# Kernel tuning notes

Hardware: AMD Instinct MI355X
Metric: run time of the kernel (lower is better)

The kernel has to match this reference:

```python
import jax, jax.numpy as jnp
import numpy as np

D_MODEL = 1024
NUM_HEADS = 16
HEAD_DIM = D_MODEL // NUM_HEADS
B, S = 4, 2048


def _xavier(key, shape, gain=0.1):
    fan_in, fan_out = shape[1], shape[0]
    a = gain * np.sqrt(6.0 / (fan_in + fan_out))
    return jax.random.uniform(key, shape, jnp.float32, -a, a)


def setup_inputs() -> dict:
    key = jax.random.key(0)
    ks = jax.random.split(key, 11)
    inp = {
        "q": jax.random.normal(ks[0], (B, S, D_MODEL), jnp.float32),
        "k": jax.random.normal(ks[1], (B, S, D_MODEL), jnp.float32),
        "v": jax.random.normal(ks[2], (B, S, D_MODEL), jnp.float32),
        # nn.Linear weights are [out, in]; y = x @ W.T + b
        "Wq": _xavier(ks[3], (D_MODEL, D_MODEL)),
        "bq": jnp.zeros((D_MODEL,), jnp.float32),
        "Wk": _xavier(ks[4], (D_MODEL, D_MODEL)),
        "bk": jnp.zeros((D_MODEL,), jnp.float32),
        "Wv": _xavier(ks[5], (D_MODEL, D_MODEL)),
        "bv": jnp.zeros((D_MODEL,), jnp.float32),
        "Wo": _xavier(ks[6], (D_MODEL, D_MODEL)),
        "bo": jnp.zeros((D_MODEL,), jnp.float32),
    }
    return inp


def reference(q, k, v, Wq, bq, Wk, bk, Wv, bv, Wo, bo):
    b = q.shape[0]
    qh = (q @ Wq.T + bq).reshape(b, -1, NUM_HEADS, HEAD_DIM).transpose(0, 2, 1, 3)
    kh = (k @ Wk.T + bk).reshape(b, -1, NUM_HEADS, HEAD_DIM).transpose(0, 2, 1, 3)
    vh = (v @ Wv.T + bv).reshape(b, -1, NUM_HEADS, HEAD_DIM).transpose(0, 2, 1, 3)
    # NOTE: original (buggy) module scales by sqrt(d_model), not sqrt(head_dim)
    scale = 1.0 / jnp.sqrt(jnp.float32(D_MODEL))
    scores = jnp.einsum('bhqd,bhkd->bhqk', qh, kh) * scale  # [B,H,S,S]
    attn = jax.nn.softmax(scores, axis=-1)
    out = jnp.einsum('bhqk,bhkd->bhqd', attn, vh)
    out = out.transpose(0, 2, 1, 3).reshape(b, -1, D_MODEL)
    return out @ Wo.T + bo
```

## Files before the change

kernel.cpp:

```cpp
#include <hip/hip_runtime.h>

typedef unsigned short u16;
typedef short bf16x8 __attribute__((ext_vector_type(8)));
typedef float f32x4 __attribute__((ext_vector_type(4)));
typedef u16 u16x8 __attribute__((ext_vector_type(8)));

__device__ __forceinline__ u16 f2bf(float f) {
  unsigned u = __float_as_uint(f);
  u = u + 0x7fffu + ((u >> 16) & 1u);
  return (u16)(u >> 16);
}

__device__ __forceinline__ float fexp2(float x) {
#if __has_builtin(__builtin_amdgcn_exp2f)
  return __builtin_amdgcn_exp2f(x);
#else
  return exp2f(x);
#endif
}

#define GLD16(ldsp, gp)                                                         \
  __builtin_amdgcn_global_load_lds(                                             \
      (__attribute__((address_space(1))) void*)(void*)(gp),                     \
      (__attribute__((address_space(3))) void*)(ldsp), 16, 0, 0)

#define CVTPK(dst, lo, hi)                                                      \
  asm("v_cvt_pk_bf16_f32 %0, %1, %2" : "=v"(dst) : "v"(lo), "v"(hi))
#define PACK8(dst, a0, a1, a2, a3, a4, a5, a6, a7)                              \
  do {                                                                          \
    union { unsigned u_[4]; bf16x8 v_; } c_;                                    \
    CVTPK(c_.u_[0], a0, a1); CVTPK(c_.u_[1], a2, a3);                           \
    CVTPK(c_.u_[2], a4, a5); CVTPK(c_.u_[3], a6, a7);                           \
    dst = c_.v_;                                                                \
  } while (0)

__global__ __launch_bounds__(256) void pack_w4(const float* __restrict__ w0,
                                               const float* __restrict__ w1,
                                               const float* __restrict__ w2,
                                               const float* __restrict__ w3,
                                               u16* __restrict__ out) {
  int i = blockIdx.x * 256 + threadIdx.x;
  int which = i >> 17;
  const float* src = which == 0 ? w0 : which == 1 ? w1 : which == 2 ? w2 : w3;
  int j = i & 131071;
  const float4* p = (const float4*)src + (size_t)j * 2;
  float4 a = p[0], b = p[1];
  u16x8 r;
  r[0] = f2bf(a.x); r[1] = f2bf(a.y); r[2] = f2bf(a.z); r[3] = f2bf(a.w);
  r[4] = f2bf(b.x); r[5] = f2bf(b.y); r[6] = f2bf(b.z); r[7] = f2bf(b.w);
  *(u16x8*)(out + (size_t)i * 8) = r;
}

__global__ __launch_bounds__(256, 4)
void gemm_qkv(const float* __restrict__ qi, const float* __restrict__ ki,
              const float* __restrict__ vi, const u16* __restrict__ wbf,
              const float* __restrict__ bq, const float* __restrict__ bk,
              const float* __restrict__ bv, u16* __restrict__ qo,
              u16* __restrict__ ko, u16* __restrict__ vo) {
  constexpr int K = 1024;
  __shared__ __align__(16) u16 As[128 * 64];
  __shared__ __align__(16) u16 Bs[128 * 64];
  const int z = blockIdx.z;
  const float* Af = z == 0 ? qi : z == 1 ? ki : vi;
  const u16* Bw = wbf + ((size_t)z << 20);
  const float* bias = z == 0 ? bq : z == 1 ? bk : bv;

  const int t = threadIdx.x;
  const int w = t >> 6, l = t & 63;
  const int lr = l & 15, lg = l >> 4;
  const int flat = blockIdx.x | (blockIdx.y << 3);
  const int swz = ((flat & 7) << 6) | (flat >> 3);
  const int row0 = (swz >> 3) * 128, col0 = (swz & 7) * 128;
  const int wm = (w >> 1) * 64, wn = (w & 1) * 64;

  f32x4 acc[4][4] = {};

  const int ar = t >> 3;
  const int xw = ((t & 7) ^ (ar & 7)) * 16;
  const float* gA = Af + (size_t)(row0 + ar) * K + (t & 7) * 8;
  const u16* gB = Bw + (size_t)(col0 + ar) * K + (((t & 7) ^ (ar & 7)) * 8);
  u16* lB = &Bs[w * 512];

  float4 a0[4], a1[4];
#pragma unroll
  for (int j = 0; j < 4; ++j) {
    const float* p = gA + (size_t)j * 32 * K;
    a0[j] = *(const float4*)p;
    a1[j] = *(const float4*)(p + 4);
  }

  for (int kt = 0; kt < 16; ++kt) {
#pragma unroll
    for (int j = 0; j < 4; ++j)
      GLD16(lB + j * 2048, gB + (size_t)j * 32 * K + kt * 64);
#pragma unroll
    for (int j = 0; j < 4; ++j) {
      bf16x8 c;
      PACK8(c, a0[j].x, a0[j].y, a0[j].z, a0[j].w, a1[j].x, a1[j].y, a1[j].z, a1[j].w);
      *(bf16x8*)((char*)As + (ar + j * 32) * 128 + xw) = c;
    }
    __syncthreads();
    if (kt < 15) {
#pragma unroll
      for (int j = 0; j < 4; ++j) {
        const float* p = gA + (size_t)j * 32 * K + (kt + 1) * 64;
        a0[j] = *(const float4*)p;
        a1[j] = *(const float4*)(p + 4);
      }
    }
#pragma unroll
    for (int kh2 = 0; kh2 < 2; ++kh2) {
      bf16x8 aF[4], bF[4];
      const int bc = (kh2 * 64 + lg * 16) ^ ((lr & 7) * 16);
#pragma unroll
      for (int mi = 0; mi < 4; ++mi)
        aF[mi] = *(const bf16x8*)((const char*)As + (wm + mi * 16 + lr) * 128 + bc);
#pragma unroll
      for (int ni = 0; ni < 4; ++ni)
        bF[ni] = *(const bf16x8*)((const char*)Bs + (wn + ni * 16 + lr) * 128 + bc);
#pragma unroll
      for (int mi = 0; mi < 4; ++mi)
#pragma unroll
        for (int ni = 0; ni < 4; ++ni)
          acc[mi][ni] = __builtin_amdgcn_mfma_f32_16x16x32_bf16(aF[mi], bF[ni],
                                                                acc[mi][ni], 0, 0, 0);
    }
    __syncthreads();
  }

#pragma unroll
  for (int mi = 0; mi < 4; ++mi) {
#pragma unroll
    for (int ni = 0; ni < 4; ++ni) {
      const int n = col0 + wn + ni * 16 + lr;
      const float bvv = bias[n];
#pragma unroll
      for (int r = 0; r < 4; ++r) {
        const int m = row0 + wm + mi * 16 + lg * 4 + r;
        const float vv = acc[mi][ni][r] + bvv;
        const int bI = m >> 11, s = m & 2047, h = n >> 6, d = n & 63;
        if (z == 0) {
          qo[((size_t)((bI << 4) + h) * 2048 + s) * 64 + d] = f2bf(vv * 0.045084223f);
        } else if (z == 1) {
          ko[((size_t)((bI << 4) + h) * 2048 + s) * 64 + d] = f2bf(vv);
        } else {
          int bh = (bI << 4) + h, tile = s >> 6, kp = s & 63;
          int kM = kp >> 5, k5 = kp & 31;
          int kpp = kM * 32 + ((k5 >> 2) & 3) * 8 + (k5 >> 4) * 4 + (k5 & 3);
          int chunk = (kpp >> 3) ^ (d & 7);
          vo[((size_t)bh << 17) + tile * 4096 + d * 64 + chunk * 8 + (kpp & 7)] = f2bf(vv);
        }
      }
    }
  }
}

__global__ __launch_bounds__(256, 3)
void gemm_out(const u16* __restrict__ A, const u16* __restrict__ B,
              const float* __restrict__ bias, float* __restrict__ outp) {
  constexpr int K = 1024;
  __shared__ __align__(16) u16 As[128 * 64];
  __shared__ __align__(16) u16 Bs[128 * 64];
  const int t = threadIdx.x;
  const int w = t >> 6;
  const int l = t & 63;
  const int lr = l & 15, lg = l >> 4;
  const int flat = blockIdx.x | (blockIdx.y << 3);
  const int swz = ((flat & 7) << 6) | (flat >> 3);
  const int row0 = (swz >> 3) * 128, col0 = (swz & 7) * 128;
  const int wm = (w >> 1) * 64, wn = (w & 1) * 64;

  f32x4 acc[4][4] = {};

  const int srow = t >> 3;
  const int scol = ((t & 7) ^ (srow & 7)) * 8;
  const u16* gA = A + (size_t)(row0 + srow) * K + scol;
  const u16* gB = B + (size_t)(col0 + srow) * K + scol;
  u16* lA = &As[w * 512];
  u16* lB = &Bs[w * 512];

  for (int k0 = 0; k0 < K; k0 += 64) {
#pragma unroll
    for (int j = 0; j < 4; ++j) {
      GLD16(lA + j * 2048, gA + (size_t)j * 32 * K + k0);
      GLD16(lB + j * 2048, gB + (size_t)j * 32 * K + k0);
    }
    __syncthreads();
#pragma unroll
    for (int kh2 = 0; kh2 < 2; ++kh2) {
      bf16x8 aF[4], bF[4];
      const int bc = (kh2 * 64 + lg * 16) ^ ((lr & 7) * 16);
#pragma unroll
      for (int mi = 0; mi < 4; ++mi)
        aF[mi] = *(const bf16x8*)((const char*)As + (wm + mi * 16 + lr) * 128 + bc);
#pragma unroll
      for (int ni = 0; ni < 4; ++ni)
        bF[ni] = *(const bf16x8*)((const char*)Bs + (wn + ni * 16 + lr) * 128 + bc);
#pragma unroll
      for (int mi = 0; mi < 4; ++mi)
#pragma unroll
        for (int ni = 0; ni < 4; ++ni)
          acc[mi][ni] = __builtin_amdgcn_mfma_f32_16x16x32_bf16(aF[mi], bF[ni],
                                                                acc[mi][ni], 0, 0, 0);
    }
    __syncthreads();
  }

#pragma unroll
  for (int mi = 0; mi < 4; ++mi)
#pragma unroll
    for (int ni = 0; ni < 4; ++ni) {
      const int n = col0 + wn + ni * 16 + lr;
      const float bv = bias[n];
#pragma unroll
      for (int r = 0; r < 4; ++r) {
        const int m = row0 + wm + mi * 16 + lg * 4 + r;
        outp[(size_t)m * 1024 + n] = acc[mi][ni][r] + bv;
      }
    }
}

#define QKC(KB, D0, D1)                                                         \
  do {                                                                          \
    const char* kb_ = (const char*)(KB);                                        \
    _Pragma("unroll")                                                           \
    for (int cq = 0; cq < 4; ++cq) {                                            \
      const char* rowp_ = kb_ + (cq * 16 + lr) * 128;                           \
      bf16x8 kf0_ = *(const bf16x8*)(rowp_ + xo0);                              \
      bf16x8 kf1_ = *(const bf16x8*)(rowp_ + xo1);                              \
      f32x4 a_ = {}, b_ = {};                                                   \
      a_ = __builtin_amdgcn_mfma_f32_16x16x32_bf16(kf0_, qf[0][0], a_, 0, 0, 0);\
      a_ = __builtin_amdgcn_mfma_f32_16x16x32_bf16(kf1_, qf[0][1], a_, 0, 0, 0);\
      b_ = __builtin_amdgcn_mfma_f32_16x16x32_bf16(kf0_, qf[1][0], b_, 0, 0, 0);\
      b_ = __builtin_amdgcn_mfma_f32_16x16x32_bf16(kf1_, qf[1][1], b_, 0, 0, 0);\
      D0[cq] = a_; D1[cq] = b_;                                                 \
    }                                                                           \
  } while (0)

#define STAGEKV(KSLOT)                                                          \
  do {                                                                          \
    u16* kd_ = &Ks[KSLOT][0] + w * 512;                                         \
    u16* vd_ = &Vl[0][0] + vs * 4096 + w * 512;      \
    GLD16(kd_, gK); GLD16(kd_ + 2048, gK + 2048);                               \
    GLD16(vd_, gV); GLD16(vd_ + 2048, gV + 2048);                               \
    gK += 4096; gV += 4096;                                                     \
  } while (0)

#define SOFTPV(SIN0, SIN1)                                                      \
  do {                                                                          \
    _Pragma("unroll")                                                           \
    for (int cq = 0; cq < 4; ++cq) {                                            \
      _Pragma("unroll")                                                         \
      for (int r = 0; r < 4; ++r) {                                             \
        SIN0[cq][r] = fexp2(SIN0[cq][r]);                                       \
        SIN1[cq][r] = fexp2(SIN1[cq][r]);                                       \
      }                                                                         \
    }                                                                           \
    bf16x8 pA0_, pA1_, pB0_, pB1_;                                              \
    PACK8(pA0_, SIN0[0][0], SIN0[0][1], SIN0[0][2], SIN0[0][3],                 \
                SIN0[1][0], SIN0[1][1], SIN0[1][2], SIN0[1][3]);                \
    PACK8(pA1_, SIN0[2][0], SIN0[2][1], SIN0[2][2], SIN0[2][3],                 \
                SIN0[3][0], SIN0[3][1], SIN0[3][2], SIN0[3][3]);                \
    PACK8(pB0_, SIN1[0][0], SIN1[0][1], SIN1[0][2], SIN1[0][3],                 \
                SIN1[1][0], SIN1[1][1], SIN1[1][2], SIN1[1][3]);                \
    PACK8(pB1_, SIN1[2][0], SIN1[2][1], SIN1[2][2], SIN1[2][3],                 \
                SIN1[3][0], SIN1[3][1], SIN1[3][2], SIN1[3][3]);                \
    sm0 = __builtin_amdgcn_mfma_f32_16x16x32_bf16(pA0_, ones, sm0, 0, 0, 0);    \
    sm0 = __builtin_amdgcn_mfma_f32_16x16x32_bf16(pA1_, ones, sm0, 0, 0, 0);    \
    sm1 = __builtin_amdgcn_mfma_f32_16x16x32_bf16(pB0_, ones, sm1, 0, 0, 0);    \
    sm1 = __builtin_amdgcn_mfma_f32_16x16x32_bf16(pB1_, ones, sm1, 0, 0, 0);    \
    const char* vbb_ = (const char*)(&Vl[0][0] + vu * 4096);     \
    _Pragma("unroll")                                                           \
    for (int dc = 0; dc < 4; ++dc) {                                            \
      const char* rp_ = vbb_ + (dc * 16 + lr) * 128;                            \
      bf16x8 vA_ = *(const bf16x8*)(rp_ + xo0);                                 \
      bf16x8 vB_ = *(const bf16x8*)(rp_ + xo1);                                 \
      o0[dc] = __builtin_amdgcn_mfma_f32_16x16x32_bf16(pA0_, vA_, o0[dc], 0,0,0);\
      o0[dc] = __builtin_amdgcn_mfma_f32_16x16x32_bf16(pA1_, vB_, o0[dc], 0,0,0);\
      o1[dc] = __builtin_amdgcn_mfma_f32_16x16x32_bf16(pB0_, vA_, o1[dc], 0,0,0);\
      o1[dc] = __builtin_amdgcn_mfma_f32_16x16x32_bf16(pB1_, vB_, o1[dc], 0,0,0);\
    }                                                                           \
  } while (0)

__global__ __launch_bounds__(256, 3)
void attn_fwd(const u16* __restrict__ qh, const u16* __restrict__ kh,
              const u16* __restrict__ vp, u16* __restrict__ aout) {
  __shared__ __align__(16) u16 Ks[2][4096];
  __shared__ __align__(16) u16 Vl[3][4096];
  const int t = threadIdx.x;
  const int w = t >> 6, l = t & 63;
  const int lr = l & 15, lg = l >> 4;
  const int flat = blockIdx.x | (blockIdx.y << 4);
  const int swz = ((flat & 7) << 7) | (flat >> 3);
  const int qb = swz & 15, bh = swz >> 4;
  const int q0 = qb * 128 + w * 32;

  bf16x8 qf[2][2];
#pragma unroll
  for (int qi = 0; qi < 2; ++qi) {
    const u16* qp = qh + ((size_t)bh * 2048 + q0 + qi * 16 + lr) * 64 + lg * 8;
    qf[qi][0] = *(const bf16x8*)qp;
    qf[qi][1] = *(const bf16x8*)(qp + 32);
  }

  f32x4 o0[4] = {}, o1[4] = {};
  f32x4 sm0 = {}, sm1 = {};
  const bf16x8 ones = {16256, 16256, 16256, 16256, 16256, 16256, 16256, 16256};

  const int krow = t >> 3, kseg = t & 7;
  const u16* gK = kh + ((size_t)bh * 2048 + krow) * 64 + ((kseg ^ (krow & 7)) * 8);
  const u16* gV = vp + ((size_t)bh << 17) + t * 8;

  const int xo0 = (lg * 16) ^ ((lr & 7) * 16);
  const int xo1 = xo0 ^ 64;

  f32x4 sA0[4], sA1[4], sB0[4], sB1[4];
  int vu = 0, vs = 0;

  STAGEKV(0);
  __syncthreads();
  vs = 1;
  STAGEKV(1);
  QKC(&Ks[0][0], sA0, sA1);
  __syncthreads();
  vs = 2;

  for (int T = 0; T < 32; T += 2) {
    if (T < 30) STAGEKV(0);
    QKC(&Ks[1][0], sB0, sB1);
    SOFTPV(sA0, sA1);
    __syncthreads();
    vu = (vu == 2) ? 0 : vu + 1;
    vs = (vs == 2) ? 0 : vs + 1;

    if (T < 30) STAGEKV(1);
    if (T < 30) QKC(&Ks[0][0], sA0, sA1);
    SOFTPV(sB0, sB1);
    __syncthreads();
    vu = (vu == 2) ? 0 : vu + 1;
    vs = (vs == 2) ? 0 : vs + 1;
  }

  const int b = bh >> 4, h = bh & 15;
#pragma unroll
  for (int r = 0; r < 4; ++r) {
    const float dA = 1.f / sm0[r];
    const float dB = 1.f / sm1[r];
    const size_t rowA = (size_t)b * 2048 + q0 + lg * 4 + r;
#pragma unroll
    for (int dc = 0; dc < 4; ++dc) {
      aout[rowA * 1024 + h * 64 + dc * 16 + lr] = f2bf(o0[dc][r] * dA);
      aout[(rowA + 16) * 1024 + h * 64 + dc * 16 + lr] = f2bf(o1[dc][r] * dB);
    }
  }
}

extern "C" void kernel_launch(void* const* d_in, const int* in_sizes, int n_in,
                              void* d_out, int out_size, void* d_ws, size_t ws_size,
                              hipStream_t stream) {
  const float* q  = (const float*)d_in[0];
  const float* k  = (const float*)d_in[1];
  const float* v  = (const float*)d_in[2];
  const float* Wq = (const float*)d_in[3];
  const float* bq = (const float*)d_in[4];
  const float* Wk = (const float*)d_in[5];
  const float* bk = (const float*)d_in[6];
  const float* Wv = (const float*)d_in[7];
  const float* bv = (const float*)d_in[8];
  const float* Wo = (const float*)d_in[9];
  const float* bo = (const float*)d_in[10];

  char* ws = (char*)d_ws;
  u16* wbf  = (u16*)(ws);
  u16* aout = (u16*)(ws + (8ull << 20));
  u16* qhB  = (u16*)(ws + (24ull << 20));
  u16* khB  = (u16*)(ws + (40ull << 20));
  u16* vtB  = (u16*)(ws + (56ull << 20));

  pack_w4<<<2048, 256, 0, stream>>>(Wq, Wk, Wv, Wo, wbf);
  gemm_qkv<<<dim3(8, 64, 3), 256, 0, stream>>>(q, k, v, wbf, bq, bk, bv,
                                               qhB, khB, vtB);
  attn_fwd<<<dim3(16, 64), 256, 0, stream>>>(qhB, khB, vtB, aout);
  gemm_out<<<dim3(8, 64), 256, 0, stream>>>(aout, wbf + (3u << 20), bo,
                                            (float*)d_out);

  (void)in_sizes; (void)n_in; (void)out_size; (void)ws_size;
}
```

Baseline: 172.7 us.

## Triple-buffer K/V with explicit vmcnt waits and MFMA priority boosts

Replaces the two-slot K / three-slot V rotation, which issued the next tile's QK^T ahead of the softmax-PV step, with a uniform three-slot K/V ring. Each iteration prefetches two tiles ahead and waits with a partial s_waitcnt vmcnt before a raw s_barrier, instead of a full __syncthreads drain. It also raises wave priority around the MFMA blocks with s_setprio and drops the cross-iteration QK software pipelining. The aim is to overlap global-to-LDS loads with compute and cut barrier stalls, at the cost of more LDS per block and less ILP between QK and PV.

```diff
diff --git a/kernel.cpp b/kernel.cpp
--- a/kernel.cpp
+++ b/kernel.cpp
@@ -220,9 +220,27 @@
     }
 }
 
-#define QKC(KB, D0, D1)                                                         \
+#define STG(SLOT)                                                               \
   do {                                                                          \
-    const char* kb_ = (const char*)(KB);                                        \
+    u16* kd_ = &Ks[SLOT][0] + w * 512;                                          \
+    u16* vd_ = &Vl[SLOT][0] + w * 512;                                          \
+    GLD16(kd_, gK); GLD16(kd_ + 2048, gK + 2048);                               \
+    GLD16(vd_, gV); GLD16(vd_ + 2048, gV + 2048);                               \
+    gK += 4096; gV += 4096;                                                     \
+  } while (0)
+
+#define WAITBAR(VMSTR)                                                          \
+  do {                                                                          \
+    asm volatile("s_waitcnt " VMSTR ::: "memory");                              \
+    __builtin_amdgcn_s_barrier();                                               \
+    __builtin_amdgcn_sched_barrier(0);                                          \
+  } while (0)
+
+#define BODYC(S)                                                                \
+  do {                                                                          \
+    const char* kb_ = (const char*)&Ks[S][0];                                   \
+    f32x4 s0_[4], s1_[4];                                                       \
+    __builtin_amdgcn_s_setprio(1);                                              \
     _Pragma("unroll")                                                           \
     for (int cq = 0; cq < 4; ++cq) {                                            \
       const char* rowp_ = kb_ + (cq * 16 + lr) * 128;                           \
@@ -233,43 +251,32 @@
       a_ = __builtin_amdgcn_mfma_f32_16x16x32_bf16(kf1_, qf[0][1], a_, 0, 0, 0);\
       b_ = __builtin_amdgcn_mfma_f32_16x16x32_bf16(kf0_, qf[1][0], b_, 0, 0, 0);\
       b_ = __builtin_amdgcn_mfma_f32_16x16x32_bf16(kf1_, qf[1][1], b_, 0, 0, 0);\
-      D0[cq] = a_; D1[cq] = b_;                                                 \
+      s0_[cq] = a_; s1_[cq] = b_;                                               \
     }                                                                           \
-  } while (0)
-
-#define STAGEKV(KSLOT)                                                          \
-  do {                                                                          \
-    u16* kd_ = &Ks[KSLOT][0] + w * 512;                                         \
-    u16* vd_ = &Vl[0][0] + vs * 4096 + w * 512;      \
-    GLD16(kd_, gK); GLD16(kd_ + 2048, gK + 2048);                               \
-    GLD16(vd_, gV); GLD16(vd_ + 2048, gV + 2048);                               \
-    gK += 4096; gV += 4096;                                                     \
-  } while (0)
-
-#define SOFTPV(SIN0, SIN1)                                                      \
-  do {                                                                          \
+    __builtin_amdgcn_s_setprio(0);                                              \
     _Pragma("unroll")                                                           \
     for (int cq = 0; cq < 4; ++cq) {                                            \
       _Pragma("unroll")                                                         \
       for (int r = 0; r < 4; ++r) {                                             \
-        SIN0[cq][r] = fexp2(SIN0[cq][r]);                                       \
-        SIN1[cq][r] = fexp2(SIN1[cq][r]);                                       \
+        s0_[cq][r] = fexp2(s0_[cq][r]);                                         \
+        s1_[cq][r] = fexp2(s1_[cq][r]);                                         \
       }                                                                         \
     }                                                                           \
     bf16x8 pA0_, pA1_, pB0_, pB1_;                                              \
-    PACK8(pA0_, SIN0[0][0], SIN0[0][1], SIN0[0][2], SIN0[0][3],                 \
-                SIN0[1][0], SIN0[1][1], SIN0[1][2], SIN0[1][3]);                \
-    PACK8(pA1_, SIN0[2][0], SIN0[2][1], SIN0[2][2], SIN0[2][3],                 \
-                SIN0[3][0], SIN0[3][1], SIN0[3][2], SIN0[3][3]);                \
-    PACK8(pB0_, SIN1[0][0], SIN1[0][1], SIN1[0][2], SIN1[0][3],                 \
-                SIN1[1][0], SIN1[1][1], SIN1[1][2], SIN1[1][3]);                \
-    PACK8(pB1_, SIN1[2][0], SIN1[2][1], SIN1[2][2], SIN1[2][3],                 \
-                SIN1[3][0], SIN1[3][1], SIN1[3][2], SIN1[3][3]);                \
+    PACK8(pA0_, s0_[0][0], s0_[0][1], s0_[0][2], s0_[0][3],                     \
+                s0_[1][0], s0_[1][1], s0_[1][2], s0_[1][3]);                    \
+    PACK8(pA1_, s0_[2][0], s0_[2][1], s0_[2][2], s0_[2][3],                     \
+                s0_[3][0], s0_[3][1], s0_[3][2], s0_[3][3]);                    \
+    PACK8(pB0_, s1_[0][0], s1_[0][1], s1_[0][2], s1_[0][3],                     \
+                s1_[1][0], s1_[1][1], s1_[1][2], s1_[1][3]);                    \
+    PACK8(pB1_, s1_[2][0], s1_[2][1], s1_[2][2], s1_[2][3],                     \
+                s1_[3][0], s1_[3][1], s1_[3][2], s1_[3][3]);                    \
+    __builtin_amdgcn_s_setprio(1);                                              \
     sm0 = __builtin_amdgcn_mfma_f32_16x16x32_bf16(pA0_, ones, sm0, 0, 0, 0);    \
     sm0 = __builtin_amdgcn_mfma_f32_16x16x32_bf16(pA1_, ones, sm0, 0, 0, 0);    \
     sm1 = __builtin_amdgcn_mfma_f32_16x16x32_bf16(pB0_, ones, sm1, 0, 0, 0);    \
     sm1 = __builtin_amdgcn_mfma_f32_16x16x32_bf16(pB1_, ones, sm1, 0, 0, 0);    \
-    const char* vbb_ = (const char*)(&Vl[0][0] + vu * 4096);     \
+    const char* vbb_ = (const char*)&Vl[S][0];                                  \
     _Pragma("unroll")                                                           \
     for (int dc = 0; dc < 4; ++dc) {                                            \
       const char* rp_ = vbb_ + (dc * 16 + lr) * 128;                            \
@@ -280,12 +287,13 @@
       o1[dc] = __builtin_amdgcn_mfma_f32_16x16x32_bf16(pB0_, vA_, o1[dc], 0,0,0);\
       o1[dc] = __builtin_amdgcn_mfma_f32_16x16x32_bf16(pB1_, vB_, o1[dc], 0,0,0);\
     }                                                                           \
+    __builtin_amdgcn_s_setprio(0);                                              \
   } while (0)
 
 __global__ __launch_bounds__(256, 3)
 void attn_fwd(const u16* __restrict__ qh, const u16* __restrict__ kh,
               const u16* __restrict__ vp, u16* __restrict__ aout) {
-  __shared__ __align__(16) u16 Ks[2][4096];
+  __shared__ __align__(16) u16 Ks[3][4096];
   __shared__ __align__(16) u16 Vl[3][4096];
   const int t = threadIdx.x;
   const int w = t >> 6, l = t & 63;
@@ -314,32 +322,18 @@
   const int xo0 = (lg * 16) ^ ((lr & 7) * 16);
   const int xo1 = xo0 ^ 64;
 
-  f32x4 sA0[4], sA1[4], sB0[4], sB1[4];
-  int vu = 0, vs = 0;
-
-  STAGEKV(0);
-  __syncthreads();
-  vs = 1;
-  STAGEKV(1);
-  QKC(&Ks[0][0], sA0, sA1);
-  __syncthreads();
-  vs = 2;
-
-  for (int T = 0; T < 32; T += 2) {
-    if (T < 30) STAGEKV(0);
-    QKC(&Ks[1][0], sB0, sB1);
-    SOFTPV(sA0, sA1);
-    __syncthreads();
-    vu = (vu == 2) ? 0 : vu + 1;
-    vs = (vs == 2) ? 0 : vs + 1;
-
-    if (T < 30) STAGEKV(1);
-    if (T < 30) QKC(&Ks[0][0], sA0, sA1);
-    SOFTPV(sB0, sB1);
-    __syncthreads();
-    vu = (vu == 2) ? 0 : vu + 1;
-    vs = (vs == 2) ? 0 : vs + 1;
-  }
+  STG(0);
+  STG(1);
+  WAITBAR("vmcnt(4)");
+
+  for (int b3 = 0; b3 < 30; b3 += 3) {
+    STG(2); BODYC(0); WAITBAR("vmcnt(4)");
+    STG(0); BODYC(1); WAITBAR("vmcnt(4)");
+    STG(1); BODYC(2); WAITBAR("vmcnt(4)");
+  }
+  BODYC(0);
+  WAITBAR("vmcnt(0)");
+  BODYC(1);
 
   const int b = bh >> 4, h = bh & 15;
 #pragma unroll
```

After: 169.8 us. About the same (-1.7%).
